# Optimization experiments

Measured on AMD Instinct MI355X. Metric: run time of the kernel, lower is better.

The kernel has to match this reference:

```python
import jax, jax.numpy as jnp
import numpy as np

# Uniform-scope sizes: B molecules, A atoms/mol, G fragments/mol, W map width,
# H hidden, L attention layers, S = G+1 (fg prompt row prepended per molecule)
B, A, G, W, H, L = 1024, 64, 31, 8, 512, 2
S = G + 1
DK = 32  # attention head dim (hard-coded in the module)


def _layernorm(x, g, b, eps):
    mu = jnp.mean(x, axis=-1, keepdims=True)
    var = jnp.var(x, axis=-1, keepdims=True)
    return g * (x - mu) * jax.lax.rsqrt(var + eps) + b


def setup_inputs() -> dict:
    key = jax.random.key(0)
    ks = jax.random.split(key, 16)
    s = 0.02
    return {
        "f_atom": jax.random.normal(ks[0], (B * A, H), jnp.float32),
        "f_group": jax.random.normal(ks[1], (B * G, H), jnp.float32),
        "fg": jax.random.normal(ks[2], (1, 3 * H), jnp.float32),
        "alpha": 0.1 * jnp.ones((1,), jnp.float32),
        "lr_w": jax.random.normal(ks[3], (3 * H, H), jnp.float32) * s,
        "lr_b": jnp.zeros((H,), jnp.float32),
        "wq_w": jax.random.normal(ks[4], (L, H, DK), jnp.float32) * s,
        "wq_b": jnp.zeros((L, DK), jnp.float32),
        "wk_w": jax.random.normal(ks[5], (L, H, DK), jnp.float32) * s,
        "wk_b": jnp.zeros((L, DK), jnp.float32),
        "wv_w": jax.random.normal(ks[6], (L, H, DK), jnp.float32) * s,
        "wv_b": jnp.zeros((L, DK), jnp.float32),
        "dense_w": jax.random.normal(ks[7], (L, DK, H), jnp.float32) * s,
        "dense_b": jnp.zeros((L, H), jnp.float32),
        "ln_g": jnp.ones((L, H), jnp.float32),
        "ln_b": jnp.zeros((L, H), jnp.float32),
        "lin_w": jax.random.normal(ks[8], (H, H), jnp.float32) * s,
        "lin_b": jnp.zeros((H,), jnp.float32),
        "norm_g": jnp.ones((H,), jnp.float32),
        "norm_b": jnp.zeros((H,), jnp.float32),
        "mapping": jax.random.randint(ks[9], (B * G, W), 0, A + 1, jnp.int64),
    }


def reference(f_atom, f_group, fg, alpha, lr_w, lr_b, wq_w, wq_b, wk_w, wk_b,
              wv_w, wv_b, dense_w, dense_b, ln_g, ln_b, lin_w, lin_b,
              norm_g, norm_b, mapping):
    # --- ragged gather + reduce + pad (vectorized: uniform scopes) ---
    a = f_atom.reshape(B, A, H)
    # prepend zero padding row per molecule (mapping index 0 -> zeros)
    a_pad = jnp.concatenate([jnp.zeros((B, 1, H), a.dtype), a], axis=1)  # [B,A+1,H]
    m = mapping.reshape(B, G, W)
    gathered = a_pad[jnp.arange(B)[:, None, None], m]  # [B,G,W,H]
    g = f_group.reshape(B, G, H)
    cur_g = jnp.concatenate(
        [gathered.sum(axis=2), gathered.max(axis=2), g], axis=-1)  # [B,G,3H]
    brics = jnp.concatenate(
        [jnp.broadcast_to(fg[None], (B, 1, 3 * H)), cur_g], axis=1)  # [B,S,3H]

    f_frag = jax.nn.relu(brics @ lr_w + lr_b)  # [B,S,H]

    # mask built from init_hiddens = f_frag (same for every layer)
    pm = (f_frag != 0).astype(f_frag.dtype)
    mask = jnp.einsum('bsh,bth->bst', pm, pm)  # [B,S,S]
    neg = jnp.asarray(-1e9, f_frag.dtype)
    scale = 1.0 / np.sqrt(DK)

    hs = f_frag
    attn = None
    for l in range(L):
        q = hs @ wq_w[l] + wq_b[l]
        k = hs @ wk_w[l] + wk_b[l]
        v = hs @ wv_w[l] + wv_b[l]
        scores = jnp.einsum('bsd,btd->bst', q, k) * scale
        scores = jnp.where(mask == 0, neg, scores)
        attn = jax.nn.softmax(scores, axis=-1)
        x = jnp.einsum('bst,btd->bsd', attn, v)
        dh = x @ dense_w[l] + dense_b[l]  # dropout is identity in eval
        hs = _layernorm(dh + hs, ln_g[l], ln_b[l], 1e-6)

    f_out = _layernorm(hs @ lin_w + lin_b, norm_g, norm_b, 1e-5) * alpha[0]
    return f_out[:, 0, :], attn
```

## Files before the change

kernel.cpp:

```cpp
#include <hip/hip_runtime.h>

#define B_   1024
#define A_   64
#define G_   31
#define W_   8
#define H_   512
#define L_   2
#define S_   32
#define DK_  32
#define K3H_ 1536

typedef short short8 __attribute__((ext_vector_type(8)));
typedef float floatx4 __attribute__((ext_vector_type(4)));

__device__ __forceinline__ float bf2f(unsigned short u){
  union { unsigned int i; float f; } x; x.i = ((unsigned int)u) << 16; return x.f;
}
__device__ __forceinline__ unsigned short f2bf(float f){
  union { float f; unsigned int i; } x; x.f = f;
  unsigned int u = x.i;
  return (unsigned short)((u + 0x7FFFu + ((u >> 16) & 1u)) >> 16);
}
__device__ __forceinline__ unsigned int pack2bf(float a, float b){
  return (unsigned int)f2bf(a) | ((unsigned int)f2bf(b) << 16);
}
__device__ __forceinline__ void gl_lds16(const unsigned short* g, unsigned short* l){
  __builtin_amdgcn_global_load_lds((const __attribute__((address_space(1))) unsigned int*)g,
                                   (__attribute__((address_space(3))) unsigned int*)l, 16, 0, 0);
}

__global__ __launch_bounds__(256) void prep_and_build(
    const float* __restrict__ f_atom, const float* __restrict__ f_group,
    const float* __restrict__ fg, const int* __restrict__ mapping,
    const float* __restrict__ lr_w, const float* __restrict__ lin_w,
    const float* __restrict__ wq_w, const float* __restrict__ wk_w, const float* __restrict__ wv_w,
    const float* __restrict__ dense_w,
    unsigned short* __restrict__ brics,
    unsigned short* __restrict__ lr_wT, unsigned short* __restrict__ lin_wT,
    unsigned short* __restrict__ qkvT, unsigned short* __restrict__ denseT){
  __shared__ __align__(16) float ldsf[8192];
  int bx = blockIdx.x;
  int tid = threadIdx.x;

  if (bx < 4096){
    int b = bx >> 2, qc = bx & 3;
    int kb = qc * 128;
    int wave = tid >> 6, lane = tid & 63;
    const float* fa = f_atom + (size_t)b * A_ * H_ + kb;
    #pragma unroll
    for (int j = 0; j < 8; ++j){
      int f = j*256 + tid;
      int r = f >> 5, c4v = f & 31;
      *(float4*)&ldsf[r*128 + c4v*4] = *(const float4*)(fa + (size_t)r*H_ + c4v*4);
    }
    __syncthreads();
    int c2 = lane * 2;
    #pragma unroll
    for (int q = 0; q < 8; ++q){
      int s = wave*8 + q;
      unsigned short* out = brics + (size_t)(b*32 + s) * K3H_ + kb;
      if (s == 0){
        #pragma unroll
        for (int t3 = 0; t3 < 3; ++t3){
          const float* fgp = fg + t3*512 + kb + c2;
          *(unsigned int*)(out + t3*512 + c2) = pack2bf(fgp[0], fgp[1]);
        }
      } else {
        int g = s - 1;
        const int* mp = mapping + ((size_t)(b * G_ + g)) * W_;
        int4 m0 = *(const int4*)mp;
        int4 m1 = *(const int4*)(mp + 4);
        int id[8] = {m0.x, m0.y, m0.z, m0.w, m1.x, m1.y, m1.z, m1.w};
        float sum0 = 0.f, sum1 = 0.f;
        float mx0 = -3.4e38f, mx1 = -3.4e38f;
        #pragma unroll
        for (int w = 0; w < 8; ++w){
          int r = id[w] > 0 ? id[w] - 1 : 0;
          float2 v = *(const float2*)&ldsf[r*128 + c2];
          bool z = (id[w] == 0);
          float v0 = z ? 0.f : v.x, v1 = z ? 0.f : v.y;
          sum0 += v0; sum1 += v1;
          mx0 = fmaxf(mx0, v0); mx1 = fmaxf(mx1, v1);
        }
        const float* gp = f_group + ((size_t)(b * G_ + g)) * H_ + kb + c2;
        float2 gv = *(const float2*)gp;
        *(unsigned int*)(out + c2)        = pack2bf(sum0, sum1);
        *(unsigned int*)(out + 512 + c2)  = pack2bf(mx0, mx1);
        *(unsigned int*)(out + 1024 + c2) = pack2bf(gv.x, gv.y);
      }
    }
    return;
  }

  if (bx < 4352){
    int tb = bx - 4096;
    const float* src; unsigned short* dst; int R, C;
    if (tb < 192){ src = lr_w;  dst = lr_wT;  R = 1536; C = 512; }
    else         { tb -= 192; src = lin_w; dst = lin_wT; R = 512;  C = 512; }
    int rt = tb >> 3, ct = tb & 7;
    int r16 = tid >> 4, c4 = tid & 15;
    #pragma unroll
    for (int p = 0; p < 4; ++p){
      int row = p*16 + r16;
      float4 v = *(const float4*)(src + (size_t)(rt*64 + row) * C + ct*64 + c4*4);
      ldsf[row*65 + c4*4+0] = v.x; ldsf[row*65 + c4*4+1] = v.y;
      ldsf[row*65 + c4*4+2] = v.z; ldsf[row*65 + c4*4+3] = v.w;
    }
    __syncthreads();
    int rr = tid >> 3, cc8 = tid & 7;
    #pragma unroll
    for (int p = 0; p < 2; ++p){
      int n = p*32 + rr;
      unsigned short o[8] __attribute__((aligned(16)));
      #pragma unroll
      for (int j = 0; j < 8; ++j) o[j] = f2bf(ldsf[(cc8*8 + j)*65 + n]);
      *(uint4*)(dst + (size_t)(ct*64 + n) * R + rt*64 + cc8*8) = *(const uint4*)o;
    }
    return;
  }

  int i = (bx - 4352) * 256 + tid;
  if (i < 98304){
    int k = i & 511; int t = i >> 9; int n = t & 31; int u = t >> 5;
    int p = u % 3, l = u / 3;
    const float* src = (p == 0) ? wq_w : (p == 1) ? wk_w : wv_w;
    qkvT[((size_t)((l*3+p)*S_ + n)) * H_ + k] = f2bf(src[((size_t)(l*H_ + k)) * DK_ + n]);
    return;
  }
  i -= 98304;
  if (i < 32768){
    int k = i & 31; int t = i >> 5; int n = t & 511; int l = t >> 9;
    denseT[((size_t)(l*H_ + n)) * DK_ + k] = f2bf(dense_w[((size_t)(l*DK_ + k)) * H_ + n]);
  }
}

__global__ __launch_bounds__(256) void gemm_frag(
    const unsigned short* __restrict__ brics, const unsigned short* __restrict__ wT,
    const float* __restrict__ lr_b, unsigned short* __restrict__ f_frag){
  __shared__ __align__(16) unsigned short As[128*64];
  __shared__ __align__(16) unsigned short Bs[128*64];
  int tid = threadIdx.x;
  int bx = blockIdx.x;
  int xcd = bx & 7, slot = bx >> 3;
  int mtile = xcd + 8 * (slot >> 2);
  int ntile = slot & 3;
  int rowStart = mtile * 128, colStart = ntile * 128;
  int lane = tid & 63, wave = tid >> 6;
  int m16 = lane & 15, quad = lane >> 4;
  int wm = wave >> 1, wn = wave & 1;
  floatx4 acc[4][4];
  #pragma unroll
  for (int i = 0; i < 4; ++i)
    #pragma unroll
    for (int j = 0; j < 4; ++j) acc[i][j] = (floatx4){0.f,0.f,0.f,0.f};

  int srow = tid >> 3;
  int gchunk = (tid & 7) ^ (srow & 7);
  size_t aOff[4], bOff[4];
  #pragma unroll
  for (int p = 0; p < 4; ++p){
    aOff[p] = (size_t)(rowStart + p*32 + srow) * K3H_ + gchunk*8;
    bOff[p] = (size_t)(colStart + p*32 + srow) * K3H_ + gchunk*8;
  }
  int fsw0 = ((0*4 + quad) ^ (m16 & 7)) * 8;
  int fsw1 = ((1*4 + quad) ^ (m16 & 7)) * 8;

  for (int kt = 0; kt < K3H_/64; ++kt){
    int kbase = kt * 64;
    #pragma unroll
    for (int p = 0; p < 4; ++p){
      gl_lds16(brics + aOff[p] + kbase, As + p*2048 + (size_t)tid*8);
      gl_lds16(wT    + bOff[p] + kbase, Bs + p*2048 + (size_t)tid*8);
    }
    __syncthreads();
    #pragma unroll
    for (int ks = 0; ks < 2; ++ks){
      int fsw = ks ? fsw1 : fsw0;
      short8 af[4], bfr[4];
      #pragma unroll
      for (int i = 0; i < 4; ++i){
        af[i]  = *(const short8*)(As + (wm*64 + i*16 + m16)*64 + fsw);
        bfr[i] = *(const short8*)(Bs + (wn*64 + i*16 + m16)*64 + fsw);
      }
      #pragma unroll
      for (int i = 0; i < 4; ++i)
        #pragma unroll
        for (int j = 0; j < 4; ++j)
          acc[i][j] = __builtin_amdgcn_mfma_f32_16x16x32_bf16(af[i], bfr[j], acc[i][j], 0, 0, 0);
    }
    __syncthreads();
  }
  #pragma unroll
  for (int i = 0; i < 4; ++i)
    #pragma unroll
    for (int j = 0; j < 4; ++j){
      int col = colStart + wn*64 + j*16 + m16;
      float bias = lr_b[col];
      #pragma unroll
      for (int r = 0; r < 4; ++r){
        int row = rowStart + wm*64 + i*16 + quad*4 + r;
        float v = acc[i][j][r] + bias;
        v = v > 0.f ? v : 0.f;
        f_frag[(size_t)row * H_ + col] = f2bf(v);
      }
    }
}

__global__ __launch_bounds__(256) void attn_kernel(
    const unsigned short* __restrict__ f_frag,
    const unsigned short* __restrict__ qkvT, const unsigned short* __restrict__ denseT,
    const float* __restrict__ wq_b, const float* __restrict__ wk_b, const float* __restrict__ wv_b,
    const float* __restrict__ dense_b, const float* __restrict__ ln_g, const float* __restrict__ ln_b,
    unsigned short* __restrict__ hsf, float* __restrict__ out_attn){
  const int HP = 544, TP = 40;
  __shared__ __align__(16) unsigned short hs[S_*544];
  __shared__ __align__(16) unsigned short Qs[S_*40];
  __shared__ __align__(16) unsigned short Ks[S_*40];
  __shared__ __align__(16) unsigned short Vt[S_*40];
  __shared__ __align__(16) unsigned short Ps[S_*40];
  __shared__ __align__(16) unsigned short Xs[S_*40];
  __shared__ unsigned long long pmask[S_*8];
  __shared__ unsigned int mz[S_];
  int b = blockIdx.x;
  int tid = threadIdx.x;
  int wave = tid >> 6, lane = tid & 63;
  int m16 = lane & 15, quad = lane >> 4;

  {
    int row = tid >> 3, cc = (tid & 7) * 64;
    const unsigned short* src = f_frag + ((size_t)(b * S_ + row)) * H_ + cc;
    unsigned short* dst = hs + row * HP + cc;
    #pragma unroll
    for (int k = 0; k < 64; k += 8)
      *(uint4*)(dst + k) = *(const uint4*)(src + k);
  }
  if (tid < S_) mz[tid] = 0u;
  __syncthreads();
  {
    int s = tid >> 3, w = tid & 7;
    const unsigned short* hrow = hs + s * HP + w * 64;
    unsigned long long m = 0ull;
    #pragma unroll
    for (int c = 0; c < 64; c += 8){
      short8 hv = *(const short8*)(hrow + c);
      #pragma unroll
      for (int j = 0; j < 8; ++j)
        if ((unsigned short)hv[j] != 0) m |= (1ull << (c + j));
    }
    pmask[s * 8 + w] = m;
  }
  __syncthreads();
  for (int idx = tid; idx < S_*S_; idx += 256){
    int s = idx >> 5, t2 = idx & 31;
    bool inter = false;
    #pragma unroll
    for (int w = 0; w < 8; ++w)
      inter = inter || ((pmask[s*8+w] & pmask[t2*8+w]) != 0ull);
    if (!inter) atomicOr(&mz[s], 1u << t2);
  }
  __syncthreads();

  const float scale = 0.17677669529663687f;
  for (int l = 0; l < L_; ++l){
    {
      int mt = wave >> 1, nt = wave & 1;
      floatx4 aq = {0,0,0,0}, ak = {0,0,0,0}, av = {0,0,0,0};
      const unsigned short* arow = hs + (mt*16 + m16) * HP + quad*8;
      const unsigned short* bq = qkvT + ((size_t)((l*3 + 0)*S_ + nt*16 + m16)) * H_ + quad*8;
      const unsigned short* bk = bq + (size_t)S_ * H_;
      const unsigned short* bv = bk + (size_t)S_ * H_;
      for (int k0 = 0; k0 < H_; k0 += 32){
        short8 a = *(const short8*)(arow + k0);
        aq = __builtin_amdgcn_mfma_f32_16x16x32_bf16(a, *(const short8*)(bq + k0), aq, 0,0,0);
        ak = __builtin_amdgcn_mfma_f32_16x16x32_bf16(a, *(const short8*)(bk + k0), ak, 0,0,0);
        av = __builtin_amdgcn_mfma_f32_16x16x32_bf16(a, *(const short8*)(bv + k0), av, 0,0,0);
      }
      int col = nt*16 + m16;
      float bqs = wq_b[l*DK_ + col], bks = wk_b[l*DK_ + col], bvs = wv_b[l*DK_ + col];
      #pragma unroll
      for (int r = 0; r < 4; ++r){
        int rw = mt*16 + quad*4 + r;
        Qs[rw*TP + col] = f2bf((aq[r] + bqs) * scale);
        Ks[rw*TP + col] = f2bf(ak[r] + bks);
        Vt[col*TP + rw] = f2bf(av[r] + bvs);
      }
    }
    __syncthreads();
    if (wave < 2){
      int mt = wave;
      short8 a  = *(const short8*)(Qs + (mt*16 + m16)*TP + quad*8);
      short8 b0 = *(const short8*)(Ks + m16*TP + quad*8);
      short8 b1 = *(const short8*)(Ks + (16 + m16)*TP + quad*8);
      floatx4 z = {0,0,0,0};
      floatx4 s0 = __builtin_amdgcn_mfma_f32_16x16x32_bf16(a, b0, z, 0,0,0);
      floatx4 s1 = __builtin_amdgcn_mfma_f32_16x16x32_bf16(a, b1, z, 0,0,0);
      #pragma unroll
      for (int r = 0; r < 4; ++r){
        int s = mt*16 + quad*4 + r;
        unsigned int m = mz[s];
        float v0 = ((m >> m16) & 1u) ? -1e9f : s0[r];
        float v1 = ((m >> (16 + m16)) & 1u) ? -1e9f : s1[r];
        float mx = fmaxf(v0, v1);
        #pragma unroll
        for (int d = 1; d < 16; d <<= 1) mx = fmaxf(mx, __shfl_xor(mx, d));
        float e0 = __expf(v0 - mx), e1 = __expf(v1 - mx);
        float sm = e0 + e1;
        #pragma unroll
        for (int d = 1; d < 16; d <<= 1) sm += __shfl_xor(sm, d);
        float inv = 1.f / sm;
        float p0 = e0 * inv, p1 = e1 * inv;
        Ps[s*TP + m16] = f2bf(p0);
        Ps[s*TP + 16 + m16] = f2bf(p1);
        if (l == L_ - 1){
          float* oa = out_attn + ((size_t)b * S_ + s) * S_;
          oa[m16] = p0; oa[16 + m16] = p1;
        }
      }
    }
    __syncthreads();
    {
      int mt = wave >> 1, nt = wave & 1;
      short8 a  = *(const short8*)(Ps + (mt*16 + m16)*TP + quad*8);
      short8 bv = *(const short8*)(Vt + (nt*16 + m16)*TP + quad*8);
      floatx4 z = {0,0,0,0};
      floatx4 x = __builtin_amdgcn_mfma_f32_16x16x32_bf16(a, bv, z, 0,0,0);
      #pragma unroll
      for (int r = 0; r < 4; ++r)
        Xs[(mt*16 + quad*4 + r)*TP + nt*16 + m16] = f2bf(x[r]);
    }
    __syncthreads();
    {
      short8 bx0 = *(const short8*)(Xs + m16*TP + quad*8);
      short8 bx1 = *(const short8*)(Xs + (16 + m16)*TP + quad*8);
      #pragma unroll
      for (int j = 0; j < 8; ++j){
        int dct = wave*8 + j;
        short8 aw = *(const short8*)(denseT + ((size_t)(l*H_ + dct*16 + m16)) * DK_ + quad*8);
        floatx4 z = {0,0,0,0};
        floatx4 d0 = __builtin_amdgcn_mfma_f32_16x16x32_bf16(aw, bx0, z, 0,0,0);
        floatx4 d1 = __builtin_amdgcn_mfma_f32_16x16x32_bf16(aw, bx1, z, 0,0,0);
        int dc0 = dct*16 + quad*4;
        float4 db4 = *(const float4*)(dense_b + l*H_ + dc0);
        const float dbr[4] = {db4.x, db4.y, db4.z, db4.w};
        unsigned short* h0 = hs + m16*HP + dc0;
        unsigned short* h1 = hs + (16 + m16)*HP + dc0;
        unsigned long long u0 = *(unsigned long long*)h0;
        unsigned long long u1 = *(unsigned long long*)h1;
        unsigned long long o0 = 0ull, o1 = 0ull;
        #pragma unroll
        for (int r = 0; r < 4; ++r){
          float hv0 = bf2f((unsigned short)(u0 >> (16*r)));
          float hv1 = bf2f((unsigned short)(u1 >> (16*r)));
          o0 |= (unsigned long long)f2bf(d0[r] + dbr[r] + hv0) << (16*r);
          o1 |= (unsigned long long)f2bf(d1[r] + dbr[r] + hv1) << (16*r);
        }
        *(unsigned long long*)h0 = o0;
        *(unsigned long long*)h1 = o1;
      }
    }
    __syncthreads();
    {
      #pragma unroll
      for (int rr = 0; rr < 8; ++rr){
        int row = wave*8 + rr;
        unsigned short* hrow = hs + row*HP + lane*8;
        short8 hv = *(const short8*)hrow;
        float v[8]; float s1 = 0.f, s2 = 0.f;
        #pragma unroll
        for (int j = 0; j < 8; ++j){ v[j] = bf2f((unsigned short)hv[j]); s1 += v[j]; s2 += v[j]*v[j]; }
        #pragma unroll
        for (int d = 1; d < 64; d <<= 1){ s1 += __shfl_xor(s1, d); s2 += __shfl_xor(s2, d); }
        float mean = s1 * (1.f/512.f);
        float var = s2 * (1.f/512.f) - mean*mean;
        float rs = rsqrtf(var + 1e-6f);
        unsigned short o[8] __attribute__((aligned(16)));
        #pragma unroll
        for (int j = 0; j < 8; ++j){
          int colj = lane*8 + j;
          float nv = (v[j] - mean) * rs * ln_g[l*H_ + colj] + ln_b[l*H_ + colj];
          o[j] = f2bf(nv);
        }
        *(uint4*)hrow = *(const uint4*)o;
      }
    }
    __syncthreads();
  }
  if (tid < 64){
    *(uint4*)(hsf + (size_t)b * H_ + tid*8) = *(const uint4*)(hs + tid*8);
  }
}

__global__ __launch_bounds__(256) void final_kernel(
    const unsigned short* __restrict__ hsf, const unsigned short* __restrict__ lin_wT,
    const float* __restrict__ lin_b, const float* __restrict__ norm_g, const float* __restrict__ norm_b,
    const float* __restrict__ alpha, float* __restrict__ out_f){
  const int HP = 544;
  __shared__ __align__(16) unsigned short hsb[32*544];
  int blk = blockIdx.x;
  int tid = threadIdx.x;
  int wave = tid >> 6, lane = tid & 63;
  int m16 = lane & 15, quad = lane >> 4;
  {
    int row = tid >> 3, cc = (tid & 7) * 64;
    const unsigned short* src = hsf + ((size_t)(blk*32 + row)) * H_ + cc;
    unsigned short* dst = hsb + row*HP + cc;
    #pragma unroll
    for (int k = 0; k < 64; k += 8)
      *(uint4*)(dst + k) = *(const uint4*)(src + k);
  }
  __syncthreads();
  floatx4 acc[2][8];
  #pragma unroll
  for (int mt = 0; mt < 2; ++mt)
    #pragma unroll
    for (int j = 0; j < 8; ++j) acc[mt][j] = (floatx4){0.f,0.f,0.f,0.f};
  for (int k0 = 0; k0 < H_; k0 += 32){
    short8 a0 = *(const short8*)(hsb + m16*HP + k0 + quad*8);
    short8 a1 = *(const short8*)(hsb + (16 + m16)*HP + k0 + quad*8);
    #pragma unroll
    for (int j = 0; j < 8; ++j){
      int n = (wave*8 + j)*16 + m16;
      short8 bw = *(const short8*)(lin_wT + (size_t)n * H_ + k0 + quad*8);
      acc[0][j] = __builtin_amdgcn_mfma_f32_16x16x32_bf16(a0, bw, acc[0][j], 0,0,0);
      acc[1][j] = __builtin_amdgcn_mfma_f32_16x16x32_bf16(a1, bw, acc[1][j], 0,0,0);
    }
  }
  __syncthreads();
  #pragma unroll
  for (int mt = 0; mt < 2; ++mt)
    #pragma unroll
    for (int j = 0; j < 8; ++j){
      int col = (wave*8 + j)*16 + m16;
      float lb = lin_b[col];
      #pragma unroll
      for (int r = 0; r < 4; ++r){
        int row = mt*16 + quad*4 + r;
        hsb[row*HP + col] = f2bf(acc[mt][j][r] + lb);
      }
    }
  __syncthreads();
  float al = alpha[0];
  #pragma unroll
  for (int rr = 0; rr < 8; ++rr){
    int row = wave*8 + rr;
    const unsigned short* hrow = hsb + row*HP + lane*8;
    short8 hv = *(const short8*)hrow;
    float v[8]; float s1 = 0.f, s2 = 0.f;
    #pragma unroll
    for (int j = 0; j < 8; ++j){ v[j] = bf2f((unsigned short)hv[j]); s1 += v[j]; s2 += v[j]*v[j]; }
    #pragma unroll
    for (int d = 1; d < 64; d <<= 1){ s1 += __shfl_xor(s1, d); s2 += __shfl_xor(s2, d); }
    float mean = s1 * (1.f/512.f);
    float var = s2 * (1.f/512.f) - mean*mean;
    float rs = rsqrtf(var + 1e-5f);
    float o[8];
    #pragma unroll
    for (int j = 0; j < 8; ++j){
      int colj = lane*8 + j;
      o[j] = ((v[j] - mean) * rs * norm_g[colj] + norm_b[colj]) * al;
    }
    float* op = out_f + ((size_t)(blk*32 + row)) * H_ + lane*8;
    float4 f0 = {o[0], o[1], o[2], o[3]};
    float4 f1 = {o[4], o[5], o[6], o[7]};
    *(float4*)op = f0;
    *(float4*)(op + 4) = f1;
  }
}

extern "C" void kernel_launch(void* const* d_in, const int* in_sizes, int n_in,
                              void* d_out, int out_size, void* d_ws, size_t ws_size,
                              hipStream_t stream){
  const float* f_atom  = (const float*)d_in[0];
  const float* f_group = (const float*)d_in[1];
  const float* fg      = (const float*)d_in[2];
  const float* alpha   = (const float*)d_in[3];
  const float* lr_w    = (const float*)d_in[4];
  const float* lr_b    = (const float*)d_in[5];
  const float* wq_w    = (const float*)d_in[6];
  const float* wq_b    = (const float*)d_in[7];
  const float* wk_w    = (const float*)d_in[8];
  const float* wk_b    = (const float*)d_in[9];
  const float* wv_w    = (const float*)d_in[10];
  const float* wv_b    = (const float*)d_in[11];
  const float* dense_w = (const float*)d_in[12];
  const float* dense_b = (const float*)d_in[13];
  const float* ln_g    = (const float*)d_in[14];
  const float* ln_b    = (const float*)d_in[15];
  const float* lin_w   = (const float*)d_in[16];
  const float* lin_b   = (const float*)d_in[17];
  const float* norm_g  = (const float*)d_in[18];
  const float* norm_b  = (const float*)d_in[19];
  const int*   mapping = (const int*)d_in[20];

  unsigned short* brics  = (unsigned short*)d_ws;
  unsigned short* f_frag = brics  + (size_t)32768 * 1536;
  unsigned short* lr_wT  = f_frag + (size_t)32768 * 512;
  unsigned short* qkvT   = lr_wT  + (size_t)512 * 1536;
  unsigned short* denseT = qkvT   + (size_t)2*3*32*512;
  unsigned short* lin_wT = denseT + (size_t)2*512*32;
  unsigned short* hsf    = lin_wT + (size_t)512*512;

  float* out_f    = (float*)d_out;
  float* out_attn = out_f + (size_t)B_ * H_;

  prep_and_build<<<4864, 256, 0, stream>>>(f_atom, f_group, fg, mapping,
                                           lr_w, lin_w, wq_w, wk_w, wv_w, dense_w,
                                           brics, lr_wT, lin_wT, qkvT, denseT);
  gemm_frag<<<(32768/128) * (512/128), 256, 0, stream>>>(brics, lr_wT, lr_b, f_frag);
  attn_kernel<<<B_, 256, 0, stream>>>(f_frag, qkvT, denseT, wq_b, wk_b, wv_b,
                                      dense_b, ln_g, ln_b, hsf, out_attn);
  final_kernel<<<B_/32, 256, 0, stream>>>(hsf, lin_wT, lin_b, norm_g, norm_b, alpha, out_f);
}
```

Before: 464.7 us.

## Split brics build into separate gather, group-copy and fg blocks with 512 threads

Restructures prep_and_build to run 512-thread blocks. The atom gather blocks now write only the sum and max sections. The f_group conversion and the fg prompt rows move into their own block ranges, which removes the s==0 divergent branch and load imbalance inside the gather waves. It also changes the LDS row pitch from 544 to 552 in the attention and final kernels to alter bank mapping. The risks are idle half-blocks in the transpose path and more blocks overall.

```diff
diff --git a/kernel.cpp b/kernel.cpp
--- a/kernel.cpp
+++ b/kernel.cpp
@@ -29,7 +29,7 @@
                                    (__attribute__((address_space(3))) unsigned int*)l, 16, 0, 0);
 }
 
-__global__ __launch_bounds__(256) void prep_and_build(
+__global__ __launch_bounds__(512) void prep_and_build(
     const float* __restrict__ f_atom, const float* __restrict__ f_group,
     const float* __restrict__ fg, const int* __restrict__ mapping,
     const float* __restrict__ lr_w, const float* __restrict__ lin_w,
@@ -48,78 +48,99 @@
     int wave = tid >> 6, lane = tid & 63;
     const float* fa = f_atom + (size_t)b * A_ * H_ + kb;
     #pragma unroll
-    for (int j = 0; j < 8; ++j){
-      int f = j*256 + tid;
+    for (int j = 0; j < 4; ++j){
+      int f = j*512 + tid;
       int r = f >> 5, c4v = f & 31;
       *(float4*)&ldsf[r*128 + c4v*4] = *(const float4*)(fa + (size_t)r*H_ + c4v*4);
     }
     __syncthreads();
     int c2 = lane * 2;
     #pragma unroll
-    for (int q = 0; q < 8; ++q){
-      int s = wave*8 + q;
+    for (int q = 0; q < 4; ++q){
+      int s = wave*4 + q;
+      if (s == 0) continue;
+      int g = s - 1;
       unsigned short* out = brics + (size_t)(b*32 + s) * K3H_ + kb;
-      if (s == 0){
-        #pragma unroll
-        for (int t3 = 0; t3 < 3; ++t3){
-          const float* fgp = fg + t3*512 + kb + c2;
-          *(unsigned int*)(out + t3*512 + c2) = pack2bf(fgp[0], fgp[1]);
-        }
-      } else {
-        int g = s - 1;
-        const int* mp = mapping + ((size_t)(b * G_ + g)) * W_;
-        int4 m0 = *(const int4*)mp;
-        int4 m1 = *(const int4*)(mp + 4);
-        int id[8] = {m0.x, m0.y, m0.z, m0.w, m1.x, m1.y, m1.z, m1.w};
-        float sum0 = 0.f, sum1 = 0.f;
-        float mx0 = -3.4e38f, mx1 = -3.4e38f;
-        #pragma unroll
-        for (int w = 0; w < 8; ++w){
-          int r = id[w] > 0 ? id[w] - 1 : 0;
-          float2 v = *(const float2*)&ldsf[r*128 + c2];
-          bool z = (id[w] == 0);
-          float v0 = z ? 0.f : v.x, v1 = z ? 0.f : v.y;
-          sum0 += v0; sum1 += v1;
-          mx0 = fmaxf(mx0, v0); mx1 = fmaxf(mx1, v1);
-        }
-        const float* gp = f_group + ((size_t)(b * G_ + g)) * H_ + kb + c2;
-        float2 gv = *(const float2*)gp;
-        *(unsigned int*)(out + c2)        = pack2bf(sum0, sum1);
-        *(unsigned int*)(out + 512 + c2)  = pack2bf(mx0, mx1);
-        *(unsigned int*)(out + 1024 + c2) = pack2bf(gv.x, gv.y);
-      }
+      const int* mp = mapping + ((size_t)(b * G_ + g)) * W_;
+      int4 m0 = *(const int4*)mp;
+      int4 m1 = *(const int4*)(mp + 4);
+      int id[8] = {m0.x, m0.y, m0.z, m0.w, m1.x, m1.y, m1.z, m1.w};
+      float sum0 = 0.f, sum1 = 0.f;
+      float mx0 = -3.4e38f, mx1 = -3.4e38f;
+      #pragma unroll
+      for (int w = 0; w < 8; ++w){
+        int r = id[w] > 0 ? id[w] - 1 : 0;
+        float2 v = *(const float2*)&ldsf[r*128 + c2];
+        bool z = (id[w] == 0);
+        float v0 = z ? 0.f : v.x, v1 = z ? 0.f : v.y;
+        sum0 += v0; sum1 += v1;
+        mx0 = fmaxf(mx0, v0); mx1 = fmaxf(mx1, v1);
+      }
+      *(unsigned int*)(out + c2)       = pack2bf(sum0, sum1);
+      *(unsigned int*)(out + 512 + c2) = pack2bf(mx0, mx1);
     }
     return;
   }
 
-  if (bx < 4352){
-    int tb = bx - 4096;
+  if (bx < 8064){
+    int pair = (bx - 4096) * 8 + (tid >> 6);
+    int c0 = (tid & 63) * 8;
+    int b = pair / G_, g = pair - b * G_;
+    const float* src = f_group + (size_t)pair * H_ + c0;
+    float4 v0 = *(const float4*)src;
+    float4 v1 = *(const float4*)(src + 4);
+    unsigned short o[8] __attribute__((aligned(16)));
+    o[0]=f2bf(v0.x); o[1]=f2bf(v0.y); o[2]=f2bf(v0.z); o[3]=f2bf(v0.w);
+    o[4]=f2bf(v1.x); o[5]=f2bf(v1.y); o[6]=f2bf(v1.z); o[7]=f2bf(v1.w);
+    *(uint4*)(brics + (size_t)(b*32 + g + 1) * K3H_ + 1024 + c0) = *(const uint4*)o;
+    return;
+  }
+
+  if (bx < 8448){
+    int e = (bx - 8064) * 4096 + tid * 8;
+    int batch = e / K3H_, c = e - batch * K3H_;
+    const float* src = fg + c;
+    float4 v0 = *(const float4*)src;
+    float4 v1 = *(const float4*)(src + 4);
+    unsigned short o[8] __attribute__((aligned(16)));
+    o[0]=f2bf(v0.x); o[1]=f2bf(v0.y); o[2]=f2bf(v0.z); o[3]=f2bf(v0.w);
+    o[4]=f2bf(v1.x); o[5]=f2bf(v1.y); o[6]=f2bf(v1.z); o[7]=f2bf(v1.w);
+    *(uint4*)(brics + (size_t)batch*32*K3H_ + c) = *(const uint4*)o;
+    return;
+  }
+
+  if (bx < 8704){
+    int tb = bx - 8448;
     const float* src; unsigned short* dst; int R, C;
     if (tb < 192){ src = lr_w;  dst = lr_wT;  R = 1536; C = 512; }
     else         { tb -= 192; src = lin_w; dst = lin_wT; R = 512;  C = 512; }
     int rt = tb >> 3, ct = tb & 7;
-    int r16 = tid >> 4, c4 = tid & 15;
-    #pragma unroll
-    for (int p = 0; p < 4; ++p){
-      int row = p*16 + r16;
-      float4 v = *(const float4*)(src + (size_t)(rt*64 + row) * C + ct*64 + c4*4);
-      ldsf[row*65 + c4*4+0] = v.x; ldsf[row*65 + c4*4+1] = v.y;
-      ldsf[row*65 + c4*4+2] = v.z; ldsf[row*65 + c4*4+3] = v.w;
-    }
-    __syncthreads();
-    int rr = tid >> 3, cc8 = tid & 7;
-    #pragma unroll
-    for (int p = 0; p < 2; ++p){
-      int n = p*32 + rr;
-      unsigned short o[8] __attribute__((aligned(16)));
-      #pragma unroll
-      for (int j = 0; j < 8; ++j) o[j] = f2bf(ldsf[(cc8*8 + j)*65 + n]);
-      *(uint4*)(dst + (size_t)(ct*64 + n) * R + rt*64 + cc8*8) = *(const uint4*)o;
+    if (tid < 256){
+      int r16 = tid >> 4, c4 = tid & 15;
+      #pragma unroll
+      for (int p = 0; p < 4; ++p){
+        int row = p*16 + r16;
+        float4 v = *(const float4*)(src + (size_t)(rt*64 + row) * C + ct*64 + c4*4);
+        ldsf[row*65 + c4*4+0] = v.x; ldsf[row*65 + c4*4+1] = v.y;
+        ldsf[row*65 + c4*4+2] = v.z; ldsf[row*65 + c4*4+3] = v.w;
+      }
+    }
+    __syncthreads();
+    if (tid < 256){
+      int rr = tid >> 3, cc8 = tid & 7;
+      #pragma unroll
+      for (int p = 0; p < 2; ++p){
+        int n = p*32 + rr;
+        unsigned short o[8] __attribute__((aligned(16)));
+        #pragma unroll
+        for (int j = 0; j < 8; ++j) o[j] = f2bf(ldsf[(cc8*8 + j)*65 + n]);
+        *(uint4*)(dst + (size_t)(ct*64 + n) * R + rt*64 + cc8*8) = *(const uint4*)o;
+      }
     }
     return;
   }
 
-  int i = (bx - 4352) * 256 + tid;
+  int i = (bx - 8704) * 512 + tid;
   if (i < 98304){
     int k = i & 511; int t = i >> 9; int n = t & 31; int u = t >> 5;
     int p = u % 3, l = u / 3;
@@ -212,8 +233,8 @@
     const float* __restrict__ wq_b, const float* __restrict__ wk_b, const float* __restrict__ wv_b,
     const float* __restrict__ dense_b, const float* __restrict__ ln_g, const float* __restrict__ ln_b,
     unsigned short* __restrict__ hsf, float* __restrict__ out_attn){
-  const int HP = 544, TP = 40;
-  __shared__ __align__(16) unsigned short hs[S_*544];
+  const int HP = 552, TP = 40;
+  __shared__ __align__(16) unsigned short hs[S_*552];
   __shared__ __align__(16) unsigned short Qs[S_*40];
   __shared__ __align__(16) unsigned short Ks[S_*40];
   __shared__ __align__(16) unsigned short Vt[S_*40];
@@ -394,8 +415,8 @@
     const unsigned short* __restrict__ hsf, const unsigned short* __restrict__ lin_wT,
     const float* __restrict__ lin_b, const float* __restrict__ norm_g, const float* __restrict__ norm_b,
     const float* __restrict__ alpha, float* __restrict__ out_f){
-  const int HP = 544;
-  __shared__ __align__(16) unsigned short hsb[32*544];
+  const int HP = 552;
+  __shared__ __align__(16) unsigned short hsb[32*552];
   int blk = blockIdx.x;
   int tid = threadIdx.x;
   int wave = tid >> 6, lane = tid & 63;
@@ -503,7 +524,7 @@
   float* out_f    = (float*)d_out;
   float* out_attn = out_f + (size_t)B_ * H_;
 
-  prep_and_build<<<4864, 256, 0, stream>>>(f_atom, f_group, fg, mapping,
+  prep_and_build<<<8960, 512, 0, stream>>>(f_atom, f_group, fg, mapping,
                                            lr_w, lin_w, wq_w, wk_w, wv_w, dense_w,
                                            brics, lr_wT, lin_wT, qkvT, denseT);
   gemm_frag<<<(32768/128) * (512/128), 256, 0, stream>>>(brics, lr_wT, lr_b, f_frag);
```

After: 456.2 us. Within noise of the previous version (-1.8%).
